# Performance work log

Measured on AMD Instinct MI355X. Metric: run time of the kernel, lower is better.

## Reference

```python
import jax, jax.numpy as jnp
import numpy as np

B, L, C = 8, 3136, 384
H_, W_ = 56, 56
WS, SS, NH = 7, 3, 12
HID, AD, SD = 1536, 16, 48  # mlp hidden, Bi_direct adapter dim, dim//scale_factor


def _rpi(w):
    # relative position index, [N, N] int
    coords = np.stack(np.meshgrid(np.arange(w), np.arange(w), indexing='ij')).reshape(2, -1)
    rc = (coords[:, :, None] - coords[:, None, :]).transpose(1, 2, 0)
    rc[:, :, 0] += w - 1
    rc[:, :, 1] += w - 1
    rc[:, :, 0] *= 2 * w - 1
    return rc.sum(-1)


def _shift_mask(Hp, Wp, w, s):
    # [nW, N, N] float mask with 0 / -100, as in the torch code
    img = np.zeros((1, Hp, Wp, 1), np.float32)
    cnt = 0
    sl = (slice(0, -w), slice(-w, -s), slice(-s, None))
    for h in sl:
        for v in sl:
            img[:, h, v, :] = cnt
            cnt += 1
    mw = img.reshape(1, Hp // w, w, Wp // w, w, 1).transpose(0, 1, 3, 2, 4, 5).reshape(-1, w * w)
    am = mw[:, None, :] - mw[:, :, None]
    return np.where(am != 0, np.float32(-100.0), np.float32(0.0))


def _ln(x, g, b, eps=1e-5):
    m = x.mean(-1, keepdims=True)
    v = ((x - m) ** 2).mean(-1, keepdims=True)
    return (x - m) * jax.lax.rsqrt(v + eps) * g + b


def _wpart(x, w):
    b, h, ww, c = x.shape
    return x.reshape(b, h // w, w, ww // w, w, c).transpose(0, 1, 3, 2, 4, 5).reshape(-1, w, w, c)


def _wrev(win, w, h, ww):
    b = win.shape[0] // (h * ww // w // w)
    return win.reshape(b, h // w, ww // w, w, w, -1).transpose(0, 1, 3, 2, 4, 5).reshape(b, h, ww, -1)


def _attn(xw, w_qkv, b_qkv, w_proj, b_proj, rpb, rpi, mask):
    B_, N, c = xw.shape
    d = c // NH
    scale = d ** -0.5
    qkv = (xw @ w_qkv + b_qkv).reshape(B_, N, 3, NH, d).transpose(2, 0, 3, 1, 4)
    q, k, v = qkv[0] * scale, qkv[1], qkv[2]  # [B_, NH, N, d]
    a = jnp.einsum('bhnd,bhmd->bhnm', q, k)
    bias = rpb[rpi.reshape(-1)].reshape(N, N, NH).transpose(2, 0, 1)
    a = a + bias[None]
    if mask is not None:
        nW = mask.shape[0]
        a = (a.reshape(B_ // nW, nW, NH, N, N) + mask[None, :, None]).reshape(B_, NH, N, N)
    a = jax.nn.softmax(a, axis=-1)
    out = jnp.einsum('bhnm,bhmd->bhnd', a, v).transpose(0, 2, 1, 3).reshape(B_, N, c)
    return out @ w_proj + b_proj


def setup_inputs() -> dict:
    key = jax.random.key(0)
    ks = iter(jax.random.split(key, 24))
    r = lambda shape: jax.random.normal(next(ks), shape, jnp.float32) * 0.02
    inp = dict(
        x_FMAG=jax.random.normal(next(ks), (B, L, C), jnp.float32),
        x=jax.random.normal(next(ks), (B, L, C), jnp.float32),
        z=jax.random.normal(next(ks), (B, L, C), jnp.float32),
        mask_z=1,
        ln1_g=jnp.ones(C), ln1_b=jnp.zeros(C),
        ln2_g=jnp.ones(C), ln2_b=jnp.zeros(C),
        w_qkv=r((C, 3 * C)), b_qkv=jnp.zeros(3 * C),
        w_proj=r((C, C)), b_proj=jnp.zeros(C),
        rpb=r(((2 * WS - 1) ** 2, NH)),
        w_fc1=r((C, HID)), b_fc1=jnp.zeros(HID),
        w_fc2=r((HID, C)), b_fc2=jnp.zeros(C),
        st_dw=r((C, SD)), st_db=jnp.zeros(SD), st_uw=r((SD, C)), st_ub=jnp.zeros(C),
        t_dw=r((C, AD)), t_db=jnp.zeros(AD), t_uw=r((AD, C)), t_ub=jnp.zeros(C),
        t2_dw=r((C, AD)), t2_db=jnp.zeros(AD), t2_uw=r((AD, C)), t2_ub=jnp.zeros(C),
    )
    return inp


def reference(x_FMAG, x, z, mask_z, ln1_g, ln1_b, ln2_g, ln2_b, w_qkv, b_qkv, w_proj, b_proj, rpb,
              w_fc1, b_fc1, w_fc2, b_fc2, st_dw, st_db, st_uw, st_ub,
              t_dw, t_db, t_uw, t_ub, t2_dw, t2_db, t2_uw, t2_ub):
    rpi = jnp.asarray(_rpi(WS))
    gelu = lambda y: jax.nn.gelu(y, approximate=False)
    # adapter_st (Single_adapter_s): bottleneck with GELU
    x = gelu(x_FMAG @ st_dw + st_db) @ st_uw + st_ub + x
    shortcut_x = x
    xn = _ln(x, ln1_g, ln1_b).reshape(B, H_, W_, C)
    # x branch: NO pre-shift (faithful to source), no mask, but rolled +shift after
    xw = _wpart(xn, WS).reshape(-1, WS * WS, C)
    awx = _attn(xw, w_qkv, b_qkv, w_proj, b_proj, rpb, rpi, None)
    awx4 = awx.reshape(-1, WS, WS, C)
    x = jnp.roll(_wrev(awx4, WS, H_, W_), (SS, SS), (1, 2)).reshape(B, L, C)
    # z branch: shifted, with shift attention mask (mask_z is not None)
    shortcut_z = z
    zn = _ln(z, ln1_g, ln1_b).reshape(B, H_, W_, C)
    sz = jnp.roll(zn, (-SS, -SS), (1, 2))
    mask = jnp.asarray(_shift_mask(H_, W_, WS, SS)) if mask_z else None
    zw = _wpart(sz, WS).reshape(-1, WS * WS, C)
    awz = _attn(zw, w_qkv, b_qkv, w_proj, b_proj, rpb, rpi, mask)
    awz4 = awz.reshape(-1, WS, WS, C)
    z = jnp.roll(_wrev(awz4, WS, H_, W_), (SS, SS), (1, 2)).reshape(B, L, C)
    # cross adapters (Bi_direct_adapter: linear down/up, no activation)
    ad_t = lambda y: (y @ t_dw + t_db) @ t_uw + t_ub
    ad_t2 = lambda y: (y @ t2_dw + t2_db) @ t2_uw + t2_ub
    x1 = shortcut_x + x + ad_t(shortcut_z)
    z1 = shortcut_z + z + ad_t(shortcut_x)
    mlp = lambda y: gelu(y @ w_fc1 + b_fc1) @ w_fc2 + b_fc2
    x2 = x1 + mlp(_ln(x1, ln2_g, ln2_b)) + ad_t2(z1)
    z2 = z1 + mlp(_ln(z1, ln2_g, ln2_b)) + ad_t2(x1)
    return (x2, awx4, z2, awz4)
```

## Files before the change

### kernel.cpp

```cpp
#include <hip/hip_runtime.h>
#include <hip/hip_bf16.h>


#define TOK 25088
#define TELEM 9633792L

typedef __attribute__((ext_vector_type(4))) float f32x4;
typedef __attribute__((ext_vector_type(8))) short bf16x8;
typedef __attribute__((address_space(3))) unsigned int as3_u32;
typedef __attribute__((address_space(1))) const unsigned int as1_u32;

__device__ __forceinline__ float ldc(const void* p, long i, int code, int bf) {
  if (code == 1 ? bf : (code == 2))
    return __bfloat162float(((const __hip_bfloat16*)p)[i]);
  return ((const float*)p)[i];
}
__device__ __forceinline__ void stAny(void* p, long i, int bf, float v) {
  if (bf) ((__hip_bfloat16*)p)[i] = __float2bfloat16(v);
  else ((float*)p)[i] = v;
}
__device__ __forceinline__ unsigned short f2b(float f) {
  __hip_bfloat16 h = __float2bfloat16(f);
  return *reinterpret_cast<unsigned short*>(&h);
}
__device__ __forceinline__ float b2f(short s) {
  return __uint_as_float(((unsigned int)(unsigned short)s) << 16);
}
__device__ __forceinline__ void ld8f(const void* p, long rowbase, int c,
                                     int code, int bf, float* o) {
  bool isb = (code == 1) ? (bf != 0) : (code == 2);
  if (isb) {
    bf16x8 v = *(const bf16x8*)((const __hip_bfloat16*)p + rowbase + c);
#pragma unroll
    for (int i = 0; i < 8; ++i) o[i] = b2f(v[i]);
  } else {
    const float* f = (const float*)p + rowbase + c;
#pragma unroll
    for (int i = 0; i < 8; ++i) o[i] = f[i];
  }
}
__device__ __forceinline__ void st8(void* p, long rowbase, int c, bool isb,
                                    const float* o) {
  if (isb) {
    bf16x8 v;
#pragma unroll
    for (int i = 0; i < 8; ++i) v[i] = (short)f2b(o[i]);
    *(bf16x8*)((__hip_bfloat16*)p + rowbase + c) = v;
  } else {
    float* f = (float*)p + rowbase + c;
#pragma unroll
    for (int i = 0; i < 8; ++i) f[i] = o[i];
  }
}

__global__ void detect_dtype(const unsigned int* __restrict__ w, int* flag) {
  __shared__ int cnt;
  if (threadIdx.x == 0) cnt = 0;
  __syncthreads();
  int local = 0;
  for (int i = threadIdx.x; i < 4096; i += blockDim.x) {
    unsigned int lo = w[i] & 0xFFFFu;
    unsigned int e = (lo >> 7) & 0xFFu;
    if ((e >= 100u && e <= 135u) || lo == 0u) local++;
  }
  atomicAdd(&cnt, local);
  __syncthreads();
  if (threadIdx.x == 0) *flag = (cnt > 2600) ? 1 : 0;
}

__global__ __launch_bounds__(256) void transpose_to_bf16(
    const void* __restrict__ in, __hip_bfloat16* __restrict__ out, int K,
    int N, const int* __restrict__ flagp) {
  int bf = *flagp;
  __shared__ float tile[32][33];
  int nb = blockIdx.x * 32, kb = blockIdx.y * 32;
  int tx = threadIdx.x & 31, ty = threadIdx.x >> 5;
#pragma unroll
  for (int r = 0; r < 32; r += 8)
    tile[ty + r][tx] = ldc(in, (long)(kb + ty + r) * N + nb + tx, 1, bf);
  __syncthreads();
#pragma unroll
  for (int r = 0; r < 32; r += 8)
    out[(long)(nb + ty + r) * K + kb + tx] = __float2bfloat16(tile[tx][ty + r]);
}

__global__ __launch_bounds__(256) void build_tab(const void* __restrict__ rpb,
                                                 float* __restrict__ tab,
                                                 const int* __restrict__ flagp) {
  int bf = *flagp;
  int idx = blockIdx.x * 256 + threadIdx.x;
  if (idx >= 48 * 2401) return;
  int m = idx % 49;
  int n = (idx / 49) % 49;
  int head = (idx / 2401) % 12;
  int cls = idx / (2401 * 12);
  int in_ = n / 7, jn = n % 7, im = m / 7, jm = m % 7;
  int ridx = (in_ - im + 6) * 13 + (jn - jm + 6);
  float v = ldc(rpb, (long)ridx * 12 + head, 1, bf);
  int whE = (cls >> 1) & 1, wwE = cls & 1;
  int rhn = whE ? (in_ < 4 ? 1 : 2) : 0;
  int rwn = wwE ? (jn < 4 ? 1 : 2) : 0;
  int rhm = whE ? (im < 4 ? 1 : 2) : 0;
  int rwm = wwE ? (jm < 4 ? 1 : 2) : 0;
  if ((rhn * 3 + rwn) != (rhm * 3 + rwm)) v -= 100.f;
  tab[idx] = v;
}

__global__ __launch_bounds__(512) void gemm_bf16(
    const __hip_bfloat16* __restrict__ A, const __hip_bfloat16* __restrict__ BT,
    const void* __restrict__ bias, void* __restrict__ C, int cmode, long coff,
    long coff2, long Msplit, int accum, int doGelu, int M, int N, int K,
    const int* __restrict__ flagp) {
  const int bf = *flagp;
  __shared__ __hip_bfloat16 As[3][256 * 32];
  __shared__ __hip_bfloat16 Bs[3][128 * 32];
  const int tid = threadIdx.x;
  const int lane = tid & 63, wave = tid >> 6;
  const int wr = wave >> 1, wc = wave & 1;

  const int gx = gridDim.x;
  long id = (long)blockIdx.y * gx + blockIdx.x;
  const long nwg = (long)gx * gridDim.y;
  {
    const long q = nwg >> 3, r = nwg & 7;
    const long xcd = id & 7, pos = id >> 3;
    id = (xcd < r) ? xcd * (q + 1) + pos : r * (q + 1) + (xcd - r) * q + pos;
  }
  const long m0 = (id / gx) * 256;
  const int n0 = (int)(id % gx) * 128;

  f32x4 acc[4][4] = {};

  const int srow = wave * 16 + (lane >> 2);
  const int scol = (lane & 3) * 8;
  const __hip_bfloat16* pA0 = A + (m0 + srow) * K + scol;
  const __hip_bfloat16* pB0 = BT + (long)(n0 + srow) * K + scol;
  const long rstepA = 128 * (long)K;
  const int ldsA0 = (wave * 16) * 32;
  const int ldsA1 = (128 + wave * 16) * 32;
  const int ldsB0 = (wave * 16) * 32;

  const int row = lane & 15;
  const int kk = (lane >> 4) * 8;
  const int nt = K / 32;

  auto stage = [&](int buf, int t) {
    const int k0 = t * 32;
    __builtin_amdgcn_global_load_lds((as1_u32*)(pA0 + k0),
                                     (as3_u32*)(&As[buf][ldsA0]), 16, 0, 0);
    __builtin_amdgcn_global_load_lds((as1_u32*)(pA0 + rstepA + k0),
                                     (as3_u32*)(&As[buf][ldsA1]), 16, 0, 0);
    __builtin_amdgcn_global_load_lds((as1_u32*)(pB0 + k0),
                                     (as3_u32*)(&Bs[buf][ldsB0]), 16, 0, 0);
  };

  stage(0, 0);
  if (nt > 1) {
    stage(1, 1);
    asm volatile("s_waitcnt vmcnt(3)" ::: "memory");
  } else {
    asm volatile("s_waitcnt vmcnt(0)" ::: "memory");
  }
  __builtin_amdgcn_sched_barrier(0);
  __builtin_amdgcn_s_barrier();

  for (int t = 0; t < nt; ++t) {
    const int cur = t % 3;
    bf16x8 af[4], bfr[4];
#pragma unroll
    for (int i = 0; i < 4; ++i)
      af[i] = *(const bf16x8*)(&As[cur][(wr * 64 + i * 16 + row) * 32 + kk]);
#pragma unroll
    for (int j = 0; j < 4; ++j)
      bfr[j] = *(const bf16x8*)(&Bs[cur][(wc * 64 + j * 16 + row) * 32 + kk]);
    if (t + 2 < nt) stage((t + 2) % 3, t + 2);
#pragma unroll
    for (int i = 0; i < 4; ++i)
#pragma unroll
      for (int j = 0; j < 4; ++j)
        acc[i][j] = __builtin_amdgcn_mfma_f32_16x16x32_bf16(af[i], bfr[j],
                                                            acc[i][j], 0, 0, 0);
    if (t + 1 < nt) {
      if (t + 2 < nt)
        asm volatile("s_waitcnt vmcnt(3)" ::: "memory");
      else
        asm volatile("s_waitcnt vmcnt(0)" ::: "memory");
      __builtin_amdgcn_sched_barrier(0);
      __builtin_amdgcn_s_barrier();
    }
  }

  const int crow = (lane >> 4) * 4;
  const int ccol = lane & 15;
#pragma unroll
  for (int i = 0; i < 4; ++i) {
#pragma unroll
    for (int r = 0; r < 4; ++r) {
      long m = m0 + wr * 64 + i * 16 + crow + r;
#pragma unroll
      for (int j = 0; j < 4; ++j) {
        int n = n0 + wc * 64 + j * 16 + ccol;
        float v = acc[i][j][r];
        if (bias) v += ldc(bias, n, 1, bf);
        if (doGelu) v = 0.5f * v * (1.f + erff(v * 0.70710678118f));
        long idx = m * (long)N + n;
        if (cmode == 0) {
          ((__hip_bfloat16*)C)[idx] = __float2bfloat16(v);
        } else {
          long odx = (m < Msplit) ? coff + idx
                                  : coff2 + (m - Msplit) * (long)N + n;
          if (accum) v += ldc(C, odx, 1, bf);
          stAny(C, odx, bf, v);
        }
      }
    }
  }
}

__global__ __launch_bounds__(256) void st_down(
    const void* __restrict__ xF, const void* __restrict__ dw,
    const void* __restrict__ db, float* __restrict__ hid,
    const int* __restrict__ flagp) {
  const int bf = *flagp;
  __shared__ __hip_bfloat16 Wd[48 * 384];
  __shared__ float Db[48];
  for (int i = threadIdx.x; i < 48 * 384; i += 256) {
    int k = i / 384, c = i % 384;
    Wd[i] = __float2bfloat16(ldc(dw, (long)c * 48 + k, 1, bf));
  }
  if (threadIdx.x < 48) Db[threadIdx.x] = ldc(db, threadIdx.x, 1, bf);
  __syncthreads();
  const long t = (long)blockIdx.x * 32 + (threadIdx.x >> 3);
  const int kg = (threadIdx.x & 7) * 6;
  float acc[6];
#pragma unroll
  for (int k = 0; k < 6; ++k) acc[k] = Db[kg + k];
  for (int c = 0; c < 384; c += 8) {
    float x8[8];
    ld8f(xF, t * 384, c, 1, bf, x8);
#pragma unroll
    for (int k = 0; k < 6; ++k) {
      bf16x8 w = *(const bf16x8*)(&Wd[(kg + k) * 384 + c]);
      float s = 0.f;
#pragma unroll
      for (int i = 0; i < 8; ++i) s += x8[i] * b2f(w[i]);
      acc[k] += s;
    }
  }
#pragma unroll
  for (int k = 0; k < 6; ++k) {
    float h = acc[k];
    hid[t * 48 + kg + k] = 0.5f * h * (1.f + erff(h * 0.70710678118f));
  }
}

__global__ __launch_bounds__(256) void st_up(
    const void* __restrict__ x_in, const float* __restrict__ hid,
    const void* __restrict__ uw, const void* __restrict__ ub,
    __hip_bfloat16* __restrict__ out, const int* __restrict__ flagp) {
  const int bf = *flagp;
  __shared__ __hip_bfloat16 Wu[48 * 384];
  __shared__ float Ub[384];
  for (int i = threadIdx.x; i < 48 * 384; i += 256)
    Wu[i] = __float2bfloat16(ldc(uw, i, 1, bf));
  for (int i = threadIdx.x; i < 384; i += 256) Ub[i] = ldc(ub, i, 1, bf);
  __syncthreads();
  const long t = (long)blockIdx.x * 16 + (threadIdx.x >> 4);
  const int c0 = (threadIdx.x & 15) * 24;
  float acc[24];
#pragma unroll
  for (int i = 0; i < 24; ++i) acc[i] = Ub[c0 + i];
#pragma unroll
  for (int b3 = 0; b3 < 3; ++b3) {
    float x8[8];
    ld8f(x_in, t * 384, c0 + b3 * 8, 1, bf, x8);
#pragma unroll
    for (int i = 0; i < 8; ++i) acc[b3 * 8 + i] += x8[i];
  }
  const float* hrow = hid + t * 48;
  for (int k = 0; k < 48; ++k) {
    float h = hrow[k];
#pragma unroll
    for (int b3 = 0; b3 < 3; ++b3) {
      bf16x8 w = *(const bf16x8*)(&Wu[k * 384 + c0 + b3 * 8]);
#pragma unroll
      for (int i = 0; i < 8; ++i) acc[b3 * 8 + i] += h * b2f(w[i]);
    }
  }
#pragma unroll
  for (int b3 = 0; b3 < 3; ++b3) st8(out, t * 384, c0 + b3 * 8, true, acc + b3 * 8);
}

__global__ __launch_bounds__(256) void ad_down(
    const void* __restrict__ inA, int cA, const void* __restrict__ inB, int cB,
    const void* __restrict__ dw, const void* __restrict__ dbias,
    float* __restrict__ hidA, float* __restrict__ hidB,
    const int* __restrict__ flagp) {
  const int bf = *flagp;
  __shared__ __hip_bfloat16 Wd[16 * 384];
  __shared__ float Db[16];
  for (int i = threadIdx.x; i < 16 * 384; i += 256) {
    int k = i / 384, c = i % 384;
    Wd[i] = __float2bfloat16(ldc(dw, (long)c * 16 + k, 1, bf));
  }
  if (threadIdx.x < 16) Db[threadIdx.x] = ldc(dbias, threadIdx.x, 1, bf);
  __syncthreads();
  const long t = (long)blockIdx.x * 32 + (threadIdx.x >> 3);
  const int kg = (threadIdx.x & 7) * 2;
  float aA[2] = {Db[kg], Db[kg + 1]};
  float aB[2] = {Db[kg], Db[kg + 1]};
  for (int c = 0; c < 384; c += 8) {
    float a8[8], b8[8];
    ld8f(inA, t * 384, c, cA, bf, a8);
    ld8f(inB, t * 384, c, cB, bf, b8);
#pragma unroll
    for (int k = 0; k < 2; ++k) {
      bf16x8 w = *(const bf16x8*)(&Wd[(kg + k) * 384 + c]);
      float sa = 0.f, sb = 0.f;
#pragma unroll
      for (int i = 0; i < 8; ++i) {
        float wf = b2f(w[i]);
        sa += a8[i] * wf;
        sb += b8[i] * wf;
      }
      aA[k] += sa;
      aB[k] += sb;
    }
  }
#pragma unroll
  for (int k = 0; k < 2; ++k) {
    hidA[t * 16 + kg + k] = aA[k];
    hidB[t * 16 + kg + k] = aB[k];
  }
}

__global__ __launch_bounds__(256) void ad_up(
    const float* __restrict__ hidA, const float* __restrict__ hidB,
    const void* __restrict__ baseX, int cbX, const void* __restrict__ baseZ,
    int cbZ, const void* __restrict__ gat, long goffX, long goffZ,
    int doGather, const void* __restrict__ uw, const void* __restrict__ ubias,
    void* __restrict__ outX, long ooffX, void* __restrict__ outZ, long ooffZ,
    int outRaw, const int* __restrict__ flagp) {
  const int bf = *flagp;
  __shared__ __hip_bfloat16 Wu[16 * 384];
  __shared__ float Ub[384];
  for (int i = threadIdx.x; i < 16 * 384; i += 256)
    Wu[i] = __float2bfloat16(ldc(uw, i, 1, bf));
  for (int i = threadIdx.x; i < 384; i += 256) Ub[i] = ldc(ubias, i, 1, bf);
  __syncthreads();
  const long t = (long)blockIdx.x * 16 + (threadIdx.x >> 4);
  const int c0 = (threadIdx.x & 15) * 24;
  long grow = 0;
  if (doGather) {
    int b = (int)(t / 3136);
    int hw = (int)(t % 3136);
    int h = hw / 56, w = hw % 56;
    int hp = (h - 3 + 56) % 56, wp = (w - 3 + 56) % 56;
    int win = b * 64 + (hp / 7) * 8 + (wp / 7);
    int n = (hp % 7) * 7 + (wp % 7);
    grow = ((long)win * 49 + n) * 384;
  }
  float ox[24], oz[24];
#pragma unroll
  for (int i = 0; i < 24; ++i) {
    ox[i] = Ub[c0 + i];
    oz[i] = Ub[c0 + i];
  }
#pragma unroll
  for (int b3 = 0; b3 < 3; ++b3) {
    float v8[8];
    ld8f(baseX, t * 384, c0 + b3 * 8, cbX, bf, v8);
#pragma unroll
    for (int i = 0; i < 8; ++i) ox[b3 * 8 + i] += v8[i];
    ld8f(baseZ, t * 384, c0 + b3 * 8, cbZ, bf, v8);
#pragma unroll
    for (int i = 0; i < 8; ++i) oz[b3 * 8 + i] += v8[i];
  }
  if (doGather) {
#pragma unroll
    for (int b3 = 0; b3 < 3; ++b3) {
      float g8[8];
      ld8f(gat, goffX + grow, c0 + b3 * 8, 1, bf, g8);
#pragma unroll
      for (int i = 0; i < 8; ++i) ox[b3 * 8 + i] += g8[i];
      ld8f(gat, goffZ + grow, c0 + b3 * 8, 1, bf, g8);
#pragma unroll
      for (int i = 0; i < 8; ++i) oz[b3 * 8 + i] += g8[i];
    }
  }
  const float* ha = hidA + t * 16;
  const float* hb = hidB + t * 16;
  for (int k = 0; k < 16; ++k) {
    float hA = ha[k], hB = hb[k];
#pragma unroll
    for (int b3 = 0; b3 < 3; ++b3) {
      bf16x8 w = *(const bf16x8*)(&Wu[k * 384 + c0 + b3 * 8]);
#pragma unroll
      for (int i = 0; i < 8; ++i) {
        float wf = b2f(w[i]);
        ox[b3 * 8 + i] += hA * wf;
        oz[b3 * 8 + i] += hB * wf;
      }
    }
  }
  const bool oisb = outRaw ? (bf != 0) : true;
#pragma unroll
  for (int b3 = 0; b3 < 3; ++b3) {
    st8(outX, ooffX + t * 384, c0 + b3 * 8, oisb, ox + b3 * 8);
    st8(outZ, ooffZ + t * 384, c0 + b3 * 8, oisb, oz + b3 * 8);
  }
}

__global__ __launch_bounds__(128) void ln_kernel(
    const void* __restrict__ X, int xc, const void* __restrict__ g,
    const void* __restrict__ b, __hip_bfloat16* __restrict__ out,
    const int* __restrict__ flagp) {
  int bf = *flagp;
  long t = blockIdx.x;
  int tid = threadIdx.x;
  float v[3];
  float s = 0.f;
#pragma unroll
  for (int r = 0; r < 3; ++r) {
    v[r] = ldc(X, t * 384 + tid + r * 128, xc, bf);
    s += v[r];
  }
  __shared__ float red[2], red2[2];
  for (int off = 32; off; off >>= 1) s += __shfl_down(s, off, 64);
  if ((tid & 63) == 0) red[tid >> 6] = s;
  __syncthreads();
  float mean = (red[0] + red[1]) * (1.f / 384.f);
  float var = 0.f;
#pragma unroll
  for (int r = 0; r < 3; ++r) {
    float d = v[r] - mean;
    var += d * d;
  }
  for (int off = 32; off; off >>= 1) var += __shfl_down(var, off, 64);
  if ((tid & 63) == 0) red2[tid >> 6] = var;
  __syncthreads();
  float rstd = rsqrtf((red2[0] + red2[1]) * (1.f / 384.f) + 1e-5f);
#pragma unroll
  for (int r = 0; r < 3; ++r) {
    int c = tid + r * 128;
    out[t * 384 + c] = __float2bfloat16((v[r] - mean) * rstd *
                                        ldc(g, c, 1, bf) + ldc(b, c, 1, bf));
  }
}

__global__ __launch_bounds__(256) void attn_mfma(
    const __hip_bfloat16* __restrict__ qkv, const float* __restrict__ tab,
    __hip_bfloat16* __restrict__ outp, const int* __restrict__ maskz) {
  __shared__ __hip_bfloat16 lds[4][64 * 72 + 32 * 72];
  const int wave = threadIdx.x >> 6, lane = threadIdx.x & 63;
  const int pair = blockIdx.x * 4 + wave;
  const int head = pair % 12;
  const int win = pair / 12;
  const int shifted = win >= 512;
  const int wn = win & 511;
  const int b = wn >> 6, wh = (wn >> 3) & 7, ww = wn & 7;
  const int useMask = shifted && (*maskz != 0);
  const int cls = useMask ? (((wh == 7) ? 2 : 0) | ((ww == 7) ? 1 : 0)) : 0;
  const float* tb = tab + (long)(cls * 12 + head) * 2401;
  __hip_bfloat16* P = lds[wave];
  __hip_bfloat16* VT = lds[wave] + 64 * 72;

  auto tokOf = [&](int n) -> long {
    n = (n < 49) ? n : 0;
    int i = n / 7, j = n % 7;
    int h = wh * 7 + i, w = ww * 7 + j;
    if (shifted) {
      h = (h + 3) % 56;
      w = (w + 3) % 56;
    }
    return (shifted ? (long)TOK : 0) + ((long)b * 56 + h) * 56 + w;
  };

  const int fr = lane & 15;
  const int fq = lane >> 4;
  bf16x8 qf[4], kf[4];
#pragma unroll
  for (int i = 0; i < 4; ++i) {
    long t = tokOf(i * 16 + fr);
    const __hip_bfloat16* basep = qkv + t * 1152 + head * 32 + fq * 8;
    qf[i] = *(const bf16x8*)(basep);
    kf[i] = *(const bf16x8*)(basep + 384);
  }
  for (int e = lane; e < 32 * 16; e += 64)
    VT[(e >> 4) * 72 + 48 + (e & 15)] = __float2bfloat16(0.f);
  for (int e = lane; e < 49 * 32; e += 64) {
    int n = e >> 5, d = e & 31;
    VT[d * 72 + n] = qkv[tokOf(n) * 1152 + 768 + head * 32 + d];
  }
  f32x4 acc[4][4] = {};
#pragma unroll
  for (int i = 0; i < 4; ++i)
#pragma unroll
    for (int j = 0; j < 4; ++j)
      acc[i][j] =
          __builtin_amdgcn_mfma_f32_16x16x32_bf16(qf[i], kf[j], acc[i][j], 0, 0, 0);
  const float scale = 0.17677669529663687f;
#pragma unroll
  for (int i = 0; i < 4; ++i) {
#pragma unroll
    for (int r = 0; r < 4; ++r) {
      int n = i * 16 + fq * 4 + r;
      float s[4];
      float mx = -1e30f;
#pragma unroll
      for (int j = 0; j < 4; ++j) {
        int m = j * 16 + fr;
        float v = acc[i][j][r] * scale;
        if (m < 49 && n < 49) v += tb[n * 49 + m];
        s[j] = (m < 49) ? v : -1e30f;
        mx = fmaxf(mx, s[j]);
      }
#pragma unroll
      for (int d = 1; d < 16; d <<= 1) mx = fmaxf(mx, __shfl_xor(mx, d));
      float sum = 0.f;
#pragma unroll
      for (int j = 0; j < 4; ++j) {
        float p = (16 * j + fr < 49) ? __expf(s[j] - mx) : 0.f;
        s[j] = p;
        sum += p;
      }
#pragma unroll
      for (int d = 1; d < 16; d <<= 1) sum += __shfl_xor(sum, d);
      float inv = 1.f / sum;
#pragma unroll
      for (int j = 0; j < 4; ++j)
        P[n * 72 + j * 16 + fr] = __float2bfloat16(s[j] * inv);
    }
  }
  f32x4 o[4][2] = {};
#pragma unroll
  for (int ks = 0; ks < 2; ++ks) {
    bf16x8 pa[4], vb[2];
#pragma unroll
    for (int i2 = 0; i2 < 4; ++i2)
      pa[i2] = *(const bf16x8*)(P + (i2 * 16 + fr) * 72 + ks * 32 + fq * 8);
#pragma unroll
    for (int j2 = 0; j2 < 2; ++j2)
      vb[j2] = *(const bf16x8*)(VT + (j2 * 16 + fr) * 72 + ks * 32 + fq * 8);
#pragma unroll
    for (int i2 = 0; i2 < 4; ++i2)
#pragma unroll
      for (int j2 = 0; j2 < 2; ++j2)
        o[i2][j2] =
            __builtin_amdgcn_mfma_f32_16x16x32_bf16(pa[i2], vb[j2], o[i2][j2], 0, 0, 0);
  }
#pragma unroll
  for (int i2 = 0; i2 < 4; ++i2) {
#pragma unroll
    for (int r = 0; r < 4; ++r) {
      int n = i2 * 16 + fq * 4 + r;
      if (n < 49) {
#pragma unroll
        for (int j2 = 0; j2 < 2; ++j2)
          outp[((long)win * 49 + n) * 384 + head * 32 + j2 * 16 + fr] =
              __float2bfloat16(o[i2][j2][r]);
      }
    }
  }
}

extern "C" void kernel_launch(void* const* d_in, const int* in_sizes, int n_in,
                              void* d_out, int out_size, void* d_ws,
                              size_t ws_size, hipStream_t stream) {
  const void* x_FMAG = d_in[0];
  const void* x_in = d_in[1];
  const void* z_in = d_in[2];
  const int* mask_z = (const int*)d_in[3];
  const void* ln1_g = d_in[4];
  const void* ln1_b = d_in[5];
  const void* ln2_g = d_in[6];
  const void* ln2_b = d_in[7];
  const void* w_qkv = d_in[8];
  const void* b_qkv = d_in[9];
  const void* w_proj = d_in[10];
  const void* b_proj = d_in[11];
  const void* rpb = d_in[12];
  const void* w_fc1 = d_in[13];
  const void* b_fc1 = d_in[14];
  const void* w_fc2 = d_in[15];
  const void* b_fc2 = d_in[16];
  const void* st_dw = d_in[17];
  const void* st_db = d_in[18];
  const void* st_uw = d_in[19];
  const void* st_ub = d_in[20];
  const void* t_dw = d_in[21];
  const void* t_db = d_in[22];
  const void* t_uw = d_in[23];
  const void* t_ub = d_in[24];
  const void* t2_dw = d_in[25];
  const void* t2_db = d_in[26];
  const void* t2_uw = d_in[27];
  const void* t2_ub = d_in[28];

  const long T = TELEM;
  char* base = (char*)d_ws;
  __hip_bfloat16* W6bf = (__hip_bfloat16*)base; base += T * 2;
  __hip_bfloat16* W7bf = (__hip_bfloat16*)base; base += T * 2;
  __hip_bfloat16* Sbf = (__hip_bfloat16*)base; base += 2 * T * 2;
  char* D = base; base += 16 * T;
  __hip_bfloat16* W0bf = (__hip_bfloat16*)D;
  __hip_bfloat16* QKVbf = (__hip_bfloat16*)(D + 2 * T);
  __hip_bfloat16* Hbf = (__hip_bfloat16*)D;
  __hip_bfloat16* TQ = (__hip_bfloat16*)base; base += 384L * 1152 * 2;
  __hip_bfloat16* TP = (__hip_bfloat16*)base; base += 384L * 384 * 2;
  __hip_bfloat16* T1 = (__hip_bfloat16*)base; base += 384L * 1536 * 2;
  __hip_bfloat16* T2 = (__hip_bfloat16*)base; base += 1536L * 384 * 2;
  float* tab = (float*)base; base += 48L * 2401 * 4;
  float* hidS = (float*)base; base += (long)TOK * 48 * 4;
  float* hidA = (float*)base; base += (long)TOK * 16 * 4;
  float* hidB = (float*)base; base += (long)TOK * 16 * 4;
  int* flag = (int*)base;

  detect_dtype<<<1, 256, 0, stream>>>((const unsigned int*)x_FMAG, flag);

  transpose_to_bf16<<<dim3(1152 / 32, 384 / 32), 256, 0, stream>>>(
      w_qkv, TQ, 384, 1152, flag);
  transpose_to_bf16<<<dim3(384 / 32, 384 / 32), 256, 0, stream>>>(
      w_proj, TP, 384, 384, flag);
  transpose_to_bf16<<<dim3(1536 / 32, 384 / 32), 256, 0, stream>>>(
      w_fc1, T1, 384, 1536, flag);
  transpose_to_bf16<<<dim3(384 / 32, 1536 / 32), 256, 0, stream>>>(
      w_fc2, T2, 1536, 384, flag);
  build_tab<<<(48 * 2401 + 255) / 256, 256, 0, stream>>>(rpb, tab, flag);

  auto gemmb = [&](const __hip_bfloat16* A, const __hip_bfloat16* BT,
                   const void* bias, void* C, int cmode, long coff, long coff2,
                   long msplit, int accum, int gelu, int M, int N, int K) {
    dim3 g(N / 128, M / 256);
    gemm_bf16<<<g, 512, 0, stream>>>(A, BT, bias, C, cmode, coff, coff2,
                                     msplit, accum, gelu, M, N, K, flag);
  };

  st_down<<<TOK / 32, 256, 0, stream>>>(x_FMAG, st_dw, st_db, hidS, flag);
  st_up<<<TOK / 16, 256, 0, stream>>>(x_in, hidS, st_uw, st_ub, W0bf, flag);
  ln_kernel<<<TOK, 128, 0, stream>>>(W0bf, 2, ln1_g, ln1_b, Sbf, flag);
  ln_kernel<<<TOK, 128, 0, stream>>>(z_in, 1, ln1_g, ln1_b, Sbf + T, flag);
  gemmb(Sbf, TQ, b_qkv, QKVbf, 0, 0, 0, 2 * TOK, 0, 0, 2 * TOK, 1152, 384);
  attn_mfma<<<1024 * 12 / 4, 256, 0, stream>>>(QKVbf, tab, Sbf, mask_z);
  gemmb(Sbf, TP, b_proj, d_out, 1, T, 3 * T, TOK, 0, 0, 2 * TOK, 384, 384);
  ad_down<<<TOK / 32, 256, 0, stream>>>(z_in, 1, W0bf, 2, t_dw, t_db, hidA,
                                        hidB, flag);
  ad_up<<<TOK / 16, 256, 0, stream>>>(hidA, hidB, W0bf, 2, z_in, 1, d_out, T,
                                      3 * T, 1, t_uw, t_ub, W6bf, 0, W7bf, 0,
                                      0, flag);
  ln_kernel<<<TOK, 128, 0, stream>>>(W6bf, 2, ln2_g, ln2_b, Sbf, flag);
  ln_kernel<<<TOK, 128, 0, stream>>>(W7bf, 2, ln2_g, ln2_b, Sbf + T, flag);
  gemmb(Sbf, T1, b_fc1, Hbf, 0, 0, 0, 2 * TOK, 0, 1, 2 * TOK, 1536, 384);
  ad_down<<<TOK / 32, 256, 0, stream>>>(W7bf, 2, W6bf, 2, t2_dw, t2_db, hidA,
                                        hidB, flag);
  ad_up<<<TOK / 16, 256, 0, stream>>>(hidA, hidB, W6bf, 2, W7bf, 2, nullptr,
                                      0, 0, 0, t2_uw, t2_ub, d_out, 0, d_out,
                                      2 * T, 1, flag);
  gemmb(Hbf, T2, b_fc2, d_out, 1, 0, 2 * T, TOK, 1, 0, 2 * TOK, 384, 1536);
}
```

Measured before the change: 1.167 ms.

## Enlarge GEMM block tile to 512 rows and use tanh GELU approximation

```diff
diff --git a/kernel.cpp b/kernel.cpp
--- a/kernel.cpp
+++ b/kernel.cpp
@@ -25,6 +25,12 @@
 }
 __device__ __forceinline__ float b2f(short s) {
   return __uint_as_float(((unsigned int)(unsigned short)s) << 16);
+}
+__device__ __forceinline__ float gelu_fast(float x) {
+  float u = x * (0.79788456f + 0.03567741f * x * x);
+  float e = __expf(2.f * u);
+  float th = 1.f - 2.f / (e + 1.f);
+  return 0.5f * x * (1.f + th);
 }
 __device__ __forceinline__ void ld8f(const void* p, long rowbase, int c,
                                      int code, int bf, float* o) {
@@ -112,11 +118,10 @@
     long coff2, long Msplit, int accum, int doGelu, int M, int N, int K,
     const int* __restrict__ flagp) {
   const int bf = *flagp;
-  __shared__ __hip_bfloat16 As[3][256 * 32];
+  __shared__ __hip_bfloat16 As[3][512 * 32];
   __shared__ __hip_bfloat16 Bs[3][128 * 32];
   const int tid = threadIdx.x;
   const int lane = tid & 63, wave = tid >> 6;
-  const int wr = wave >> 1, wc = wave & 1;
 
   const int gx = gridDim.x;
   long id = (long)blockIdx.y * gx + blockIdx.x;
@@ -126,38 +131,34 @@
     const long xcd = id & 7, pos = id >> 3;
     id = (xcd < r) ? xcd * (q + 1) + pos : r * (q + 1) + (xcd - r) * q + pos;
   }
-  const long m0 = (id / gx) * 256;
+  const long m0 = (id / gx) * 512;
   const int n0 = (int)(id % gx) * 128;
 
-  f32x4 acc[4][4] = {};
-
-  const int srow = wave * 16 + (lane >> 2);
+  f32x4 acc[4][8] = {};
+
   const int scol = (lane & 3) * 8;
-  const __hip_bfloat16* pA0 = A + (m0 + srow) * K + scol;
-  const __hip_bfloat16* pB0 = BT + (long)(n0 + srow) * K + scol;
-  const long rstepA = 128 * (long)K;
-  const int ldsA0 = (wave * 16) * 32;
-  const int ldsA1 = (128 + wave * 16) * 32;
-  const int ldsB0 = (wave * 16) * 32;
-
-  const int row = lane & 15;
+  const __hip_bfloat16* pA0 = A + (m0 + wave * 64 + (lane >> 2)) * K + scol;
+  const __hip_bfloat16* pB0 = BT + (long)(n0 + wave * 16 + (lane >> 2)) * K + scol;
+
+  const int fr = lane & 15;
   const int kk = (lane >> 4) * 8;
   const int nt = K / 32;
 
   auto stage = [&](int buf, int t) {
     const int k0 = t * 32;
-    __builtin_amdgcn_global_load_lds((as1_u32*)(pA0 + k0),
-                                     (as3_u32*)(&As[buf][ldsA0]), 16, 0, 0);
-    __builtin_amdgcn_global_load_lds((as1_u32*)(pA0 + rstepA + k0),
-                                     (as3_u32*)(&As[buf][ldsA1]), 16, 0, 0);
-    __builtin_amdgcn_global_load_lds((as1_u32*)(pB0 + k0),
-                                     (as3_u32*)(&Bs[buf][ldsB0]), 16, 0, 0);
+#pragma unroll
+    for (int i = 0; i < 4; ++i)
+      __builtin_amdgcn_global_load_lds(
+          (as1_u32*)(pA0 + k0 + (long)i * 16 * K),
+          (as3_u32*)(&As[buf][(wave * 64 + i * 16) * 32]), 16, 0, 0);
+    __builtin_amdgcn_global_load_lds(
+        (as1_u32*)(pB0 + k0), (as3_u32*)(&Bs[buf][(wave * 16) * 32]), 16, 0, 0);
   };
 
   stage(0, 0);
   if (nt > 1) {
     stage(1, 1);
-    asm volatile("s_waitcnt vmcnt(3)" ::: "memory");
+    asm volatile("s_waitcnt vmcnt(5)" ::: "memory");
   } else {
     asm volatile("s_waitcnt vmcnt(0)" ::: "memory");
   }
@@ -166,23 +167,23 @@
 
   for (int t = 0; t < nt; ++t) {
     const int cur = t % 3;
-    bf16x8 af[4], bfr[4];
+    bf16x8 af[4], bfr[8];
 #pragma unroll
     for (int i = 0; i < 4; ++i)
-      af[i] = *(const bf16x8*)(&As[cur][(wr * 64 + i * 16 + row) * 32 + kk]);
-#pragma unroll
-    for (int j = 0; j < 4; ++j)
-      bfr[j] = *(const bf16x8*)(&Bs[cur][(wc * 64 + j * 16 + row) * 32 + kk]);
+      af[i] = *(const bf16x8*)(&As[cur][(wave * 64 + i * 16 + fr) * 32 + kk]);
+#pragma unroll
+    for (int j = 0; j < 8; ++j)
+      bfr[j] = *(const bf16x8*)(&Bs[cur][(j * 16 + fr) * 32 + kk]);
     if (t + 2 < nt) stage((t + 2) % 3, t + 2);
 #pragma unroll
     for (int i = 0; i < 4; ++i)
 #pragma unroll
-      for (int j = 0; j < 4; ++j)
+      for (int j = 0; j < 8; ++j)
         acc[i][j] = __builtin_amdgcn_mfma_f32_16x16x32_bf16(af[i], bfr[j],
                                                             acc[i][j], 0, 0, 0);
     if (t + 1 < nt) {
       if (t + 2 < nt)
-        asm volatile("s_waitcnt vmcnt(3)" ::: "memory");
+        asm volatile("s_waitcnt vmcnt(5)" ::: "memory");
       else
         asm volatile("s_waitcnt vmcnt(0)" ::: "memory");
       __builtin_amdgcn_sched_barrier(0);
@@ -191,18 +192,17 @@
   }
 
   const int crow = (lane >> 4) * 4;
-  const int ccol = lane & 15;
 #pragma unroll
   for (int i = 0; i < 4; ++i) {
 #pragma unroll
     for (int r = 0; r < 4; ++r) {
-      long m = m0 + wr * 64 + i * 16 + crow + r;
-#pragma unroll
-      for (int j = 0; j < 4; ++j) {
-        int n = n0 + wc * 64 + j * 16 + ccol;
+      long m = m0 + wave * 64 + i * 16 + crow + r;
+#pragma unroll
+      for (int j = 0; j < 8; ++j) {
+        int n = n0 + j * 16 + fr;
         float v = acc[i][j][r];
         if (bias) v += ldc(bias, n, 1, bf);
-        if (doGelu) v = 0.5f * v * (1.f + erff(v * 0.70710678118f));
+        if (doGelu) v = gelu_fast(v);
         long idx = m * (long)N + n;
         if (cmode == 0) {
           ((__hip_bfloat16*)C)[idx] = __float2bfloat16(v);
@@ -631,7 +631,7 @@
   auto gemmb = [&](const __hip_bfloat16* A, const __hip_bfloat16* BT,
                    const void* bias, void* C, int cmode, long coff, long coff2,
                    long msplit, int accum, int gelu, int M, int N, int K) {
-    dim3 g(N / 128, M / 256);
+    dim3 g(N / 128, M / 512);
     gemm_bf16<<<g, 512, 0, stream>>>(A, BT, bias, C, cmode, coff, coff2,
                                      msplit, accum, gelu, M, N, K, flag);
   };
```

After: 1.555 ms. 33.2% more time.
